# Kernel tuning notes

Hardware: AMD Instinct MI355X
Metric: run time of the kernel (lower is better)

The kernel has to match this reference:

```python
import jax, jax.numpy as jnp
import numpy as np
from functools import partial

B, N, C = 32, 22743, 80          # batch, total anchors (608px: 3*(19^2+38^2+76^2)), num classes
CONF_THR = 0.05                  # cfg.THRESHOLD_PREDICT_CONF
NMS_THR = 0.5                    # cfg.THRESHOLD_PREDICT_NMS
TOPK = 1000                      # fixed-size candidate set (jit-compatible NMS)
BOX_OFFSET = 10.0                # per (image,label) coordinate offset -> batched/label NMS


def setup_inputs() -> dict:
    key = jax.random.key(0)
    k1, k2 = jax.random.split(key, 2)
    p_yolo = jax.random.normal(k1, (B, N, 5 + C), jnp.float32)
    # anchor priors: normalized cx,cy,w,h per box
    ancs = jax.random.uniform(k2, (N, 4), jnp.float32, 0.05, 0.9)
    # fsize_p: feature grid size repeated per box, exactly as np.repeat in the source
    fsizes = np.array([19.0, 38.0, 76.0], np.float32)
    nums_ceng = (fsizes ** 2 * 3).astype(np.int64)          # boxes per pyramid level
    fsize = jnp.asarray(np.repeat(fsizes, nums_ceng)[:, None] * np.ones((1, 2), np.float32))
    return {"p_yolo": p_yolo, "ancs": ancs, "fsize": fsize}


def _decode(p_yolo, ancs, fsize):
    # fix_boxes4yolo3: xy = anc_xy + sigmoid(txy)/fsize ; wh = exp(twh)*anc_wh
    xy = ancs[None, :, :2] + jax.nn.sigmoid(p_yolo[..., :2]) / fsize[None]
    wh = jnp.exp(p_yolo[..., 2:4]) * ancs[None, :, 2:4]
    ltrb = jnp.concatenate([xy - wh * 0.5, xy + wh * 0.5], axis=-1)  # xywh2ltrb
    conf = jax.nn.sigmoid(p_yolo[..., 4])
    cls = jax.nn.sigmoid(p_yolo[..., 5:])
    return ltrb, conf, cls


def _iou_matrix(b):  # b: [K,4] ltrb
    lt = jnp.maximum(b[:, None, :2], b[None, :, :2])
    rb = jnp.minimum(b[:, None, 2:], b[None, :, 2:])
    wh = jnp.clip(rb - lt, 0.0)
    inter = wh[..., 0] * wh[..., 1]
    area = (b[:, 2] - b[:, 0]) * (b[:, 3] - b[:, 1])
    return inter / (area[:, None] + area[None, :] - inter + 1e-9)


def reference(p_yolo, ancs, fsize):
    ltrb, conf, cls = _decode(p_yolo, ancs, fsize)
    boxes = ltrb.reshape(B * N, 4)
    conf = conf.reshape(B * N)
    labels = jnp.argmax(cls.reshape(B * N, C), axis=-1) + 1   # labels start at 1
    ids = jnp.repeat(jnp.arange(B, dtype=jnp.int32), N)
    valid = conf > CONF_THR                                   # mask_box
    scores = jnp.where(valid, conf, 0.0)
    # fixed-size candidate selection (replaces data-dependent torch.where gather)
    sc_k, idx = jax.lax.top_k(scores, TOPK)
    boxes_k = boxes[idx]
    labels_k = labels[idx]
    ids_k = ids[idx]
    valid_k = valid[idx]
    # label_nms: offset boxes by (image,label) key so classes/images never suppress each other
    nms_key = (ids_k * (C + 1) + labels_k).astype(jnp.float32)
    iou = _iou_matrix(boxes_k + nms_key[:, None] * BOX_OFFSET)
    rng = jnp.arange(TOPK)
    def body(i, keep):
        suppress = keep[i] & (iou[i] > NMS_THR) & (rng > i)
        return keep & ~suppress
    keep = jax.lax.fori_loop(0, TOPK, body, valid_k)
    ids2 = jnp.where(keep, ids_k, -1)
    boxes2 = jnp.where(keep[:, None], boxes_k, 0.0)
    labels2 = jnp.where(keep, labels_k, -1)
    scores2 = jnp.where(keep, sc_k, 0.0)
    return ids2, boxes2, labels2, scores2, keep
```

## Files before the change

kernel.cpp:

```cpp
#include <hip/hip_runtime.h>
#include <stdint.h>

#define B_    32
#define N_    22743
#define C_    80
#define BN    (B_ * N_)
#define TOPK_ 1000
#define CAP   16384
#define SORTN 4096


__device__ __forceinline__ float sig32(float x) {
    return (float)(1.0 / (1.0 + exp(-(double)x)));
}


__global__ void k_init(uint32_t* hist, uint32_t* ctl) {
    int t = threadIdx.x;
    if (t < 256) hist[t] = 0;
    if (t == 0) { ctl[0] = 0; ctl[1] = TOPK_; ctl[2] = 0; ctl[3] = 0; }
}

__global__ void k_scores(const float* __restrict__ p, uint32_t* __restrict__ sc) {
    int i = blockIdx.x * blockDim.x + threadIdx.x;
    if (i >= BN) return;
    float x = p[(size_t)i * 85 + 4];
    float c = sig32(x);
    float s = (c > 0.05f) ? c : 0.0f;
    sc[i] = __float_as_uint(s);
}

__global__ void k_hist(const uint32_t* __restrict__ sc, uint32_t* __restrict__ hist,
                       const uint32_t* __restrict__ ctl, int r) {
    __shared__ uint32_t sh[256];
    if (threadIdx.x < 256) sh[threadIdx.x] = 0;
    __syncthreads();
    uint32_t pref = ctl[0];
    int shPrefix = 32 - 8 * r;
    int shBin = 24 - 8 * r;
    uint64_t prefHi = (uint64_t)pref >> shPrefix;
    int stride = gridDim.x * blockDim.x;
    for (int i = blockIdx.x * blockDim.x + threadIdx.x; i < BN; i += stride) {
        uint32_t s = sc[i];
        if (((uint64_t)s >> shPrefix) == prefHi)
            atomicAdd(&sh[(s >> shBin) & 0xFFu], 1u);
    }
    __syncthreads();
    if (threadIdx.x < 256 && sh[threadIdx.x])
        atomicAdd(&hist[threadIdx.x], sh[threadIdx.x]);
}

__global__ void k_scan(uint32_t* hist, uint32_t* ctl, int r) {
    __shared__ uint32_t sh[256];
    int t = threadIdx.x;
    sh[t] = hist[t];
    __syncthreads();
    hist[t] = 0;
    if (t == 0) {
        uint32_t krem = ctl[1];
        uint32_t cum = 0;
        int b = 255;
        for (; b >= 0; --b) {
            uint32_t h = sh[b];
            if (cum + h >= krem) break;
            cum += h;
        }
        if (b < 0) b = 0;
        ctl[2] += cum;
        ctl[1] = krem - cum;
        ctl[0] |= ((uint32_t)b) << (24 - 8 * r);
    }
}

__global__ void k_compact(const uint32_t* __restrict__ sc, uint32_t* ctl,
                          unsigned long long* __restrict__ cand) {
    uint32_t T = ctl[0];
    int stride = gridDim.x * blockDim.x;
    for (int i = blockIdx.x * blockDim.x + threadIdx.x; i < BN; i += stride) {
        uint32_t s = sc[i];
        if (s >= T) {
            uint32_t pos = atomicAdd(&ctl[3], 1u);
            if (pos < CAP)
                cand[pos] = ((unsigned long long)s << 32) | (uint32_t)(~(uint32_t)i);
        }
    }
}

__global__ __launch_bounds__(1024) void k_sort(const unsigned long long* __restrict__ cand,
                                               const uint32_t* __restrict__ ctl,
                                               uint32_t* __restrict__ sel_idx,
                                               uint32_t* __restrict__ sel_sb) {
    __shared__ unsigned long long key[SORTN];
    uint32_t cnt = ctl[3];
    if (cnt > CAP) cnt = CAP;
    if (cnt > SORTN) cnt = SORTN;
    for (int t = threadIdx.x; t < SORTN; t += blockDim.x)
        key[t] = (t < (int)cnt) ? cand[t] : 0ull;
    __syncthreads();
    for (int k = 2; k <= SORTN; k <<= 1) {
        for (int j = k >> 1; j > 0; j >>= 1) {
            for (int t = threadIdx.x; t < SORTN; t += blockDim.x) {
                int ixj = t ^ j;
                if (ixj > t) {
                    unsigned long long a = key[t], b = key[ixj];
                    bool up = ((t & k) == 0);
                    if (up ? (a < b) : (a > b)) { key[t] = b; key[ixj] = a; }
                }
            }
            __syncthreads();
        }
    }
    for (int t = threadIdx.x; t < TOPK_; t += blockDim.x) {
        unsigned long long kk = key[t];
        sel_sb[t] = (uint32_t)(kk >> 32);
        sel_idx[t] = ~((uint32_t)kk);
    }
}

__global__ void k_prep(const float* __restrict__ p, const float* __restrict__ ancs,
                       const float* __restrict__ fsize,
                       const uint32_t* __restrict__ sel_idx,
                       const uint32_t* __restrict__ sel_sb,
                       float4* __restrict__ obox, float4* __restrict__ boxo,
                       float* __restrict__ area, int* __restrict__ ids,
                       int* __restrict__ labels, uint32_t* __restrict__ svalid,
                       float* __restrict__ sscore) {
    int j = blockIdx.x * blockDim.x + threadIdx.x;
    if (j >= TOPK_) return;
    uint32_t i = sel_idx[j];
    if (i >= (uint32_t)BN) i = 0;
    int b = (int)(i / (uint32_t)N_);
    int n = (int)(i - (uint32_t)b * (uint32_t)N_);
    const float* row = p + (size_t)i * 85;
    float ax = ancs[n * 4 + 0], ay = ancs[n * 4 + 1];
    float aw = ancs[n * 4 + 2], ah = ancs[n * 4 + 3];
    float fx = fsize[n * 2 + 0], fy = fsize[n * 2 + 1];
    float x = __fadd_rn(ax, __fdiv_rn(sig32(row[0]), fx));
    float y = __fadd_rn(ay, __fdiv_rn(sig32(row[1]), fy));
    float w = __fmul_rn((float)exp((double)row[2]), aw);
    float h = __fmul_rn((float)exp((double)row[3]), ah);
    float hw = __fmul_rn(w, 0.5f), hh = __fmul_rn(h, 0.5f);
    float l = __fsub_rn(x, hw), t = __fsub_rn(y, hh);
    float r = __fadd_rn(x, hw), bt = __fadd_rn(y, hh);
    float best = -1.0f; int lab = 0;
    for (int c = 0; c < C_; ++c) {
        float s = sig32(row[5 + c]);
        if (s > best) { best = s; lab = c; }
    }
    int label = lab + 1;
    float keyf = (float)(b * (C_ + 1) + label);
    float off = __fmul_rn(keyf, 10.0f);
    float4 ob = make_float4(__fadd_rn(l, off), __fadd_rn(t, off),
                            __fadd_rn(r, off), __fadd_rn(bt, off));
    obox[j] = ob;
    boxo[j] = make_float4(l, t, r, bt);
    float dx = __fsub_rn(ob.z, ob.x), dy = __fsub_rn(ob.w, ob.y);
    area[j] = __fmul_rn(dx, dy);
    ids[j] = b;
    labels[j] = label;
    float sc = __uint_as_float(sel_sb[j]);
    sscore[j] = sc;
    svalid[j] = (sc > 0.0f) ? 1u : 0u;
}

__global__ void k_mask(const float4* __restrict__ obox, const float* __restrict__ area,
                       unsigned long long* __restrict__ mask) {
    int gtid = blockIdx.x * blockDim.x + threadIdx.x;
    int wid = gtid >> 6;
    int lane = threadIdx.x & 63;
    if (wid >= TOPK_ * 16) return;
    int i = wid >> 4, c = wid & 15;
    int col = (c << 6) | lane;
    float4 bi = obox[i];
    float ai = area[i];
    bool pred = false;
    if (col < TOPK_ && col > i) {
        float4 bj = obox[col];
        float lx = fmaxf(bi.x, bj.x), ly = fmaxf(bi.y, bj.y);
        float rx = fminf(bi.z, bj.z), ry = fminf(bi.w, bj.w);
        float ww = fmaxf(__fsub_rn(rx, lx), 0.0f);
        float hh = fmaxf(__fsub_rn(ry, ly), 0.0f);
        float inter = __fmul_rn(ww, hh);
        float denom = __fadd_rn(__fsub_rn(__fadd_rn(ai, area[col]), inter), 1e-9f);
        float iou = __fdiv_rn(inter, denom);
        pred = iou > 0.5f;
    }
    unsigned long long m = __ballot(pred);
    if (lane == 0) mask[wid] = m;
}

__global__ __launch_bounds__(1024) void k_nms_out(
        const unsigned long long* __restrict__ gmask,
        const uint32_t* __restrict__ svalid,
        const float4* __restrict__ boxo,
        const int* __restrict__ ids, const int* __restrict__ labels,
        const float* __restrict__ sscore,
        float* __restrict__ out) {
    __shared__ unsigned long long smask[500 * 16];
    __shared__ unsigned long long srem[16];
    __shared__ unsigned char sval[TOPK_];
    int tid = threadIdx.x;
    for (int t = tid; t < TOPK_; t += 1024) sval[t] = (unsigned char)svalid[t];
    for (int t = tid; t < 8000; t += 1024) smask[t] = gmask[t];
    __syncthreads();
    unsigned long long removed = 0;
    if (tid < 64) {
        for (int i = 0; i < 500; ++i) {
            int w = i >> 6, bit = i & 63;
            unsigned long long rm_i = __shfl(removed, w);
            bool live = sval[i] && !((rm_i >> bit) & 1ull);
            if (live && tid < 16) removed |= smask[i * 16 + tid];
        }
    }
    __syncthreads();
    for (int t = tid; t < 8000; t += 1024) smask[t] = gmask[8000 + t];
    __syncthreads();
    if (tid < 64) {
        for (int i = 500; i < 1000; ++i) {
            int w = i >> 6, bit = i & 63;
            unsigned long long rm_i = __shfl(removed, w);
            bool live = sval[i] && !((rm_i >> bit) & 1ull);
            if (live && tid < 16) removed |= smask[(i - 500) * 16 + tid];
        }
        if (tid < 16) srem[tid] = removed;
    }
    __syncthreads();
    for (int j = tid; j < TOPK_; j += 1024) {
        bool keep = sval[j] && !((srem[j >> 6] >> (j & 63)) & 1ull);
        float4 bx = boxo[j];
        out[j]                = keep ? (float)ids[j] : -1.0f;
        out[1000 + 4 * j + 0] = keep ? bx.x : 0.0f;
        out[1000 + 4 * j + 1] = keep ? bx.y : 0.0f;
        out[1000 + 4 * j + 2] = keep ? bx.z : 0.0f;
        out[1000 + 4 * j + 3] = keep ? bx.w : 0.0f;
        out[5000 + j]         = keep ? (float)labels[j] : -1.0f;
        out[6000 + j]         = keep ? sscore[j] : 0.0f;
        out[7000 + j]         = keep ? 1.0f : 0.0f;
    }
}


extern "C" void kernel_launch(void* const* d_in, const int* in_sizes, int n_in,
                              void* d_out, int out_size, void* d_ws, size_t ws_size,
                              hipStream_t stream) {
    const float* p     = (const float*)d_in[0];
    const float* ancs  = (const float*)d_in[1];
    const float* fsize = (const float*)d_in[2];

    char* ws = (char*)d_ws;
    size_t off = 0;
    uint32_t* sc = (uint32_t*)(ws + off);                 off += (size_t)BN * 4;
    uint32_t* hist = (uint32_t*)(ws + off);               off += 1024;
    uint32_t* ctl = (uint32_t*)(ws + off);                off += 64;
    unsigned long long* cand = (unsigned long long*)(ws + off); off += (size_t)CAP * 8;
    uint32_t* sel_idx = (uint32_t*)(ws + off);            off += 4096;
    uint32_t* sel_sb = (uint32_t*)(ws + off);             off += 4096;
    float4* obox = (float4*)(ws + off);                   off += 16 * 1024;
    float4* boxo = (float4*)(ws + off);                   off += 16 * 1024;
    float* area = (float*)(ws + off);                     off += 4096;
    int* ids = (int*)(ws + off);                          off += 4096;
    int* labels = (int*)(ws + off);                       off += 4096;
    uint32_t* svalid = (uint32_t*)(ws + off);             off += 4096;
    float* sscore = (float*)(ws + off);                   off += 4096;
    unsigned long long* mask = (unsigned long long*)(ws + off); off += 16000 * 8;

    k_init<<<1, 256, 0, stream>>>(hist, ctl);
    k_scores<<<(BN + 255) / 256, 256, 0, stream>>>(p, sc);
    for (int r = 0; r < 4; ++r) {
        k_hist<<<512, 256, 0, stream>>>(sc, hist, ctl, r);
        k_scan<<<1, 256, 0, stream>>>(hist, ctl, r);
    }
    k_compact<<<512, 256, 0, stream>>>(sc, ctl, cand);
    k_sort<<<1, 1024, 0, stream>>>(cand, ctl, sel_idx, sel_sb);
    k_prep<<<4, 256, 0, stream>>>(p, ancs, fsize, sel_idx, sel_sb,
                                  obox, boxo, area, ids, labels, svalid, sscore);
    k_mask<<<4000, 256, 0, stream>>>(obox, area, mask);
    k_nms_out<<<1, 1024, 0, stream>>>(mask, svalid, boxo, ids, labels, sscore,
                                      (float*)d_out);
}
```

Before: 562.2 us.

## Cut radix passes, replace bitonic sort with rank-select, fast bitwise NMS

The init and per-round scan kernels are folded into the scores and histogram kernels; the scan now runs in the last block to finish, found with an atomic counter. Only two 8-bit radix passes are done, so the coarser threshold admits more candidates. Those are placed by a parallel rank count over up to 2048 keys instead of a single-block 4096-element bitonic sort. The mask kernel skips lower-triangle tiles, and the serial NMS becomes a single-wave pass per 64-box chunk that handles boxes with no intra-chunk conflicts in bulk. The risk is that more than 2048 candidates pass the 16-bit prefix threshold, which would silently truncate the ranking.

New measurement: 578.3 us. +2.9%, slower.

```diff
diff --git a/kernel.cpp b/kernel.cpp
--- a/kernel.cpp
+++ b/kernel.cpp
@@ -1,5 +1,7 @@
 #include <hip/hip_runtime.h>
 #include <stdint.h>
+
+typedef unsigned long long ull;
 
 #define B_    32
 #define N_    22743
@@ -7,7 +9,8 @@
 #define BN    (B_ * N_)
 #define TOPK_ 1000
 #define CAP   16384
-#define SORTN 4096
+#define RANKN 2048
+#define HBLOCKS 512
 
 
 __device__ __forceinline__ float sig32(float x) {
@@ -15,50 +18,52 @@
 }
 
 
-__global__ void k_init(uint32_t* hist, uint32_t* ctl) {
-    int t = threadIdx.x;
-    if (t < 256) hist[t] = 0;
-    if (t == 0) { ctl[0] = 0; ctl[1] = TOPK_; ctl[2] = 0; ctl[3] = 0; }
-}
-
-__global__ void k_scores(const float* __restrict__ p, uint32_t* __restrict__ sc) {
+__global__ void k_scores(const float* __restrict__ p, uint32_t* __restrict__ sc,
+                         uint32_t* __restrict__ hist, uint32_t* __restrict__ ctl) {
+    if (blockIdx.x == 0) {
+        if (threadIdx.x < 256) hist[threadIdx.x] = 0;
+        if (threadIdx.x == 0) {
+            ctl[0] = 0; ctl[1] = TOPK_; ctl[2] = 0; ctl[3] = 0; ctl[4] = 0; ctl[5] = 0;
+        }
+    }
     int i = blockIdx.x * blockDim.x + threadIdx.x;
     if (i >= BN) return;
     float x = p[(size_t)i * 85 + 4];
     float c = sig32(x);
-    float s = (c > 0.05f) ? c : 0.0f;
-    sc[i] = __float_as_uint(s);
-}
-
-__global__ void k_hist(const uint32_t* __restrict__ sc, uint32_t* __restrict__ hist,
-                       const uint32_t* __restrict__ ctl, int r) {
+    sc[i] = __float_as_uint((c > 0.05f) ? c : 0.0f);
+}
+
+__global__ __launch_bounds__(256) void k_hist(const uint32_t* __restrict__ sc,
+                                              uint32_t* hist, uint32_t* ctl, int r) {
     __shared__ uint32_t sh[256];
-    if (threadIdx.x < 256) sh[threadIdx.x] = 0;
-    __syncthreads();
-    uint32_t pref = ctl[0];
+    __shared__ int last;
+    int tid = threadIdx.x;
+    sh[tid] = 0;
+    __syncthreads();
+    uint32_t pref = r ? ctl[0] : 0u;
     int shPrefix = 32 - 8 * r;
     int shBin = 24 - 8 * r;
     uint64_t prefHi = (uint64_t)pref >> shPrefix;
     int stride = gridDim.x * blockDim.x;
-    for (int i = blockIdx.x * blockDim.x + threadIdx.x; i < BN; i += stride) {
+    for (int i = blockIdx.x * blockDim.x + tid; i < BN; i += stride) {
         uint32_t s = sc[i];
         if (((uint64_t)s >> shPrefix) == prefHi)
             atomicAdd(&sh[(s >> shBin) & 0xFFu], 1u);
     }
     __syncthreads();
-    if (threadIdx.x < 256 && sh[threadIdx.x])
-        atomicAdd(&hist[threadIdx.x], sh[threadIdx.x]);
-}
-
-__global__ void k_scan(uint32_t* hist, uint32_t* ctl, int r) {
-    __shared__ uint32_t sh[256];
-    int t = threadIdx.x;
-    sh[t] = hist[t];
-    __syncthreads();
-    hist[t] = 0;
-    if (t == 0) {
-        uint32_t krem = ctl[1];
-        uint32_t cum = 0;
+    if (sh[tid]) atomicAdd(&hist[tid], sh[tid]);
+    __threadfence();
+    if (tid == 0) {
+        uint32_t d = atomicAdd(&ctl[4 + r], 1u);
+        last = (d == gridDim.x - 1);
+    }
+    __syncthreads();
+    if (!last) return;
+    uint32_t v = atomicExch(&hist[tid], 0u);
+    sh[tid] = v;
+    __syncthreads();
+    if (tid == 0) {
+        uint32_t krem = ctl[1], cum = 0;
         int b = 255;
         for (; b >= 0; --b) {
             uint32_t h = sh[b];
@@ -68,12 +73,12 @@
         if (b < 0) b = 0;
         ctl[2] += cum;
         ctl[1] = krem - cum;
-        ctl[0] |= ((uint32_t)b) << (24 - 8 * r);
+        ctl[0] = pref | ((uint32_t)b << shBin);
     }
 }
 
 __global__ void k_compact(const uint32_t* __restrict__ sc, uint32_t* ctl,
-                          unsigned long long* __restrict__ cand) {
+                          ull* __restrict__ cand) {
     uint32_t T = ctl[0];
     int stride = gridDim.x * blockDim.x;
     for (int i = blockIdx.x * blockDim.x + threadIdx.x; i < BN; i += stride) {
@@ -81,39 +86,30 @@
         if (s >= T) {
             uint32_t pos = atomicAdd(&ctl[3], 1u);
             if (pos < CAP)
-                cand[pos] = ((unsigned long long)s << 32) | (uint32_t)(~(uint32_t)i);
-        }
-    }
-}
-
-__global__ __launch_bounds__(1024) void k_sort(const unsigned long long* __restrict__ cand,
-                                               const uint32_t* __restrict__ ctl,
-                                               uint32_t* __restrict__ sel_idx,
-                                               uint32_t* __restrict__ sel_sb) {
-    __shared__ unsigned long long key[SORTN];
-    uint32_t cnt = ctl[3];
-    if (cnt > CAP) cnt = CAP;
-    if (cnt > SORTN) cnt = SORTN;
-    for (int t = threadIdx.x; t < SORTN; t += blockDim.x)
-        key[t] = (t < (int)cnt) ? cand[t] : 0ull;
-    __syncthreads();
-    for (int k = 2; k <= SORTN; k <<= 1) {
-        for (int j = k >> 1; j > 0; j >>= 1) {
-            for (int t = threadIdx.x; t < SORTN; t += blockDim.x) {
-                int ixj = t ^ j;
-                if (ixj > t) {
-                    unsigned long long a = key[t], b = key[ixj];
-                    bool up = ((t & k) == 0);
-                    if (up ? (a < b) : (a > b)) { key[t] = b; key[ixj] = a; }
-                }
-            }
-            __syncthreads();
-        }
-    }
-    for (int t = threadIdx.x; t < TOPK_; t += blockDim.x) {
-        unsigned long long kk = key[t];
-        sel_sb[t] = (uint32_t)(kk >> 32);
-        sel_idx[t] = ~((uint32_t)kk);
+                cand[pos] = ((ull)s << 32) | (uint32_t)(~(uint32_t)i);
+        }
+    }
+}
+
+__global__ __launch_bounds__(256) void k_rank(const ull* __restrict__ cand,
+                                              const uint32_t* __restrict__ ctl,
+                                              uint32_t* __restrict__ sel_idx,
+                                              uint32_t* __restrict__ sel_sb) {
+    __shared__ ull keys[RANKN];
+    int tid = threadIdx.x;
+    uint32_t cntu = ctl[3];
+    int cnt = (cntu > RANKN) ? RANKN : (int)cntu;
+    for (int t = tid; t < cnt; t += 256) keys[t] = cand[t];
+    __syncthreads();
+    int j = blockIdx.x * 256 + tid;
+    if (j >= cnt) return;
+    ull k = keys[j];
+    int rank = 0;
+    #pragma unroll 4
+    for (int t = 0; t < cnt; ++t) rank += (keys[t] > k) ? 1 : 0;
+    if (rank < TOPK_) {
+        sel_sb[rank] = (uint32_t)(k >> 32);
+        sel_idx[rank] = ~((uint32_t)k);
     }
 }
 
@@ -164,12 +160,16 @@
 }
 
 __global__ void k_mask(const float4* __restrict__ obox, const float* __restrict__ area,
-                       unsigned long long* __restrict__ mask) {
+                       ull* __restrict__ mask) {
     int gtid = blockIdx.x * blockDim.x + threadIdx.x;
     int wid = gtid >> 6;
     int lane = threadIdx.x & 63;
     if (wid >= TOPK_ * 16) return;
     int i = wid >> 4, c = wid & 15;
+    if (((c << 6) | 63) <= i) {
+        if (lane == 0) mask[wid] = 0ull;
+        return;
+    }
     int col = (c << 6) | lane;
     float4 bi = obox[i];
     float ai = area[i];
@@ -185,48 +185,60 @@
         float iou = __fdiv_rn(inter, denom);
         pred = iou > 0.5f;
     }
-    unsigned long long m = __ballot(pred);
+    ull m = __ballot(pred);
     if (lane == 0) mask[wid] = m;
 }
 
-__global__ __launch_bounds__(1024) void k_nms_out(
-        const unsigned long long* __restrict__ gmask,
+__global__ __launch_bounds__(256) void k_nms_out(
+        const ull* __restrict__ gmask,
         const uint32_t* __restrict__ svalid,
         const float4* __restrict__ boxo,
         const int* __restrict__ ids, const int* __restrict__ labels,
         const float* __restrict__ sscore,
         float* __restrict__ out) {
-    __shared__ unsigned long long smask[500 * 16];
-    __shared__ unsigned long long srem[16];
-    __shared__ unsigned char sval[TOPK_];
+    __shared__ ull srem[16];
     int tid = threadIdx.x;
-    for (int t = tid; t < TOPK_; t += 1024) sval[t] = (unsigned char)svalid[t];
-    for (int t = tid; t < 8000; t += 1024) smask[t] = gmask[t];
-    __syncthreads();
-    unsigned long long removed = 0;
     if (tid < 64) {
-        for (int i = 0; i < 500; ++i) {
-            int w = i >> 6, bit = i & 63;
-            unsigned long long rm_i = __shfl(removed, w);
-            bool live = sval[i] && !((rm_i >> bit) & 1ull);
-            if (live && tid < 16) removed |= smask[i * 16 + tid];
-        }
-    }
-    __syncthreads();
-    for (int t = tid; t < 8000; t += 1024) smask[t] = gmask[8000 + t];
-    __syncthreads();
-    if (tid < 64) {
-        for (int i = 500; i < 1000; ++i) {
-            int w = i >> 6, bit = i & 63;
-            unsigned long long rm_i = __shfl(removed, w);
-            bool live = sval[i] && !((rm_i >> bit) & 1ull);
-            if (live && tid < 16) removed |= smask[(i - 500) * 16 + tid];
-        }
-        if (tid < 16) srem[tid] = removed;
-    }
-    __syncthreads();
-    for (int j = tid; j < TOPK_; j += 1024) {
-        bool keep = sval[j] && !((srem[j >> 6] >> (j & 63)) & 1ull);
+        int lane = tid;
+        ull acc = 0;
+        ull vw[16];
+        #pragma unroll
+        for (int c = 0; c < 16; ++c) {
+            int i = c * 64 + lane;
+            bool v = (i < TOPK_) && (svalid[i] != 0u);
+            vw[c] = __ballot(v);
+        }
+        for (int c = 0; c < 16; ++c) {
+            int i0 = c * 64;
+            int ri = i0 + lane;
+            ull mcol = (ri < TOPK_) ? gmask[(size_t)ri * 16 + c] : 0ull;
+            ull suppr = __ballot(mcol != 0ull);
+            ull vic = mcol;
+            vic |= __shfl_xor(vic, 32); vic |= __shfl_xor(vic, 16);
+            vic |= __shfl_xor(vic, 8);  vic |= __shfl_xor(vic, 4);
+            vic |= __shfl_xor(vic, 2);  vic |= __shfl_xor(vic, 1);
+            ull cur = __shfl(acc, c);
+            ull avail = vw[c] & ~cur;
+            ull danger = suppr | vic;
+            ull clean = avail & ~danger;
+            ull inter = avail & danger;
+            while (clean) {
+                int b = __ffsll(clean) - 1; clean &= clean - 1;
+                if (lane < 16) acc |= gmask[(size_t)(i0 + b) * 16 + lane];
+            }
+            while (inter) {
+                int b = __ffsll(inter) - 1; inter &= inter - 1;
+                if (!((cur >> b) & 1ull)) {
+                    cur |= __shfl(mcol, b);
+                    if (lane < 16) acc |= gmask[(size_t)(i0 + b) * 16 + lane];
+                }
+            }
+        }
+        if (lane < 16) srem[lane] = acc;
+    }
+    __syncthreads();
+    for (int j = tid; j < TOPK_; j += 256) {
+        bool keep = (svalid[j] != 0u) && !((srem[j >> 6] >> (j & 63)) & 1ull);
         float4 bx = boxo[j];
         out[j]                = keep ? (float)ids[j] : -1.0f;
         out[1000 + 4 * j + 0] = keep ? bx.x : 0.0f;
@@ -249,32 +261,29 @@
 
     char* ws = (char*)d_ws;
     size_t off = 0;
-    uint32_t* sc = (uint32_t*)(ws + off);                 off += (size_t)BN * 4;
-    uint32_t* hist = (uint32_t*)(ws + off);               off += 1024;
-    uint32_t* ctl = (uint32_t*)(ws + off);                off += 64;
-    unsigned long long* cand = (unsigned long long*)(ws + off); off += (size_t)CAP * 8;
-    uint32_t* sel_idx = (uint32_t*)(ws + off);            off += 4096;
-    uint32_t* sel_sb = (uint32_t*)(ws + off);             off += 4096;
-    float4* obox = (float4*)(ws + off);                   off += 16 * 1024;
-    float4* boxo = (float4*)(ws + off);                   off += 16 * 1024;
-    float* area = (float*)(ws + off);                     off += 4096;
-    int* ids = (int*)(ws + off);                          off += 4096;
-    int* labels = (int*)(ws + off);                       off += 4096;
-    uint32_t* svalid = (uint32_t*)(ws + off);             off += 4096;
-    float* sscore = (float*)(ws + off);                   off += 4096;
-    unsigned long long* mask = (unsigned long long*)(ws + off); off += 16000 * 8;
-
-    k_init<<<1, 256, 0, stream>>>(hist, ctl);
-    k_scores<<<(BN + 255) / 256, 256, 0, stream>>>(p, sc);
-    for (int r = 0; r < 4; ++r) {
-        k_hist<<<512, 256, 0, stream>>>(sc, hist, ctl, r);
-        k_scan<<<1, 256, 0, stream>>>(hist, ctl, r);
-    }
-    k_compact<<<512, 256, 0, stream>>>(sc, ctl, cand);
-    k_sort<<<1, 1024, 0, stream>>>(cand, ctl, sel_idx, sel_sb);
+    uint32_t* sc = (uint32_t*)(ws + off);     off += (size_t)BN * 4;
+    uint32_t* hist = (uint32_t*)(ws + off);   off += 1024;
+    uint32_t* ctl = (uint32_t*)(ws + off);    off += 64;
+    ull* cand = (ull*)(ws + off);             off += (size_t)CAP * 8;
+    uint32_t* sel_idx = (uint32_t*)(ws + off); off += 4096;
+    uint32_t* sel_sb = (uint32_t*)(ws + off);  off += 4096;
+    float4* obox = (float4*)(ws + off);       off += 16 * 1024;
+    float4* boxo = (float4*)(ws + off);       off += 16 * 1024;
+    float* area = (float*)(ws + off);         off += 4096;
+    int* ids = (int*)(ws + off);              off += 4096;
+    int* labels = (int*)(ws + off);           off += 4096;
+    uint32_t* svalid = (uint32_t*)(ws + off); off += 4096;
+    float* sscore = (float*)(ws + off);       off += 4096;
+    ull* mask = (ull*)(ws + off);             off += 16000 * 8;
+
+    k_scores<<<(BN + 255) / 256, 256, 0, stream>>>(p, sc, hist, ctl);
+    k_hist<<<HBLOCKS, 256, 0, stream>>>(sc, hist, ctl, 0);
+    k_hist<<<HBLOCKS, 256, 0, stream>>>(sc, hist, ctl, 1);
+    k_compact<<<HBLOCKS, 256, 0, stream>>>(sc, ctl, cand);
+    k_rank<<<RANKN / 256, 256, 0, stream>>>(cand, ctl, sel_idx, sel_sb);
     k_prep<<<4, 256, 0, stream>>>(p, ancs, fsize, sel_idx, sel_sb,
                                   obox, boxo, area, ids, labels, svalid, sscore);
     k_mask<<<4000, 256, 0, stream>>>(obox, area, mask);
-    k_nms_out<<<1, 1024, 0, stream>>>(mask, svalid, boxo, ids, labels, sscore,
-                                      (float*)d_out);
-}
+    k_nms_out<<<1, 256, 0, stream>>>(mask, svalid, boxo, ids, labels, sscore,
+                                     (float*)d_out);
+}
```
